# Optimization experiments

Hardware: AMD Instinct MI355X
Metric: run time of the kernel (lower is better)

## Reference

```python
import jax, jax.numpy as jnp
import numpy as np

B, S, D_IN, D_HID, D_OUT, PE_DIM = 8, 4096, 1024, 1024, 1024, 16


def sinusoidal_embeddings(batch_size, seq_len, dim):
    positions = jnp.arange(seq_len)[:, None].astype(jnp.float32)
    div_term = jnp.exp(jnp.arange(0, dim, 2).astype(jnp.float32) * (-jnp.log(10000.0) / dim))
    pe = jnp.zeros((seq_len, dim), dtype=jnp.float32)
    pe = pe.at[:, 0::2].set(jnp.sin(positions * div_term))
    pe = pe.at[:, 1::2].set(jnp.cos(positions * div_term))
    return jnp.broadcast_to(pe, (batch_size, seq_len, dim))


def setup_inputs() -> dict:
    key = jax.random.key(0)
    ks = jax.random.split(key, 8)
    d_cat = D_IN + PE_DIM
    # a_logit drawn so that sigmoid(a_logit) lands in the stable decay range [0.9, 0.999]
    u = jax.random.uniform(ks[1], (D_HID,), minval=0.9, maxval=0.999)
    a_logit = jnp.log(u) - jnp.log1p(-u)  # logit
    scale_in = 1.0 / np.sqrt(d_cat)
    scale_h = 1.0 / np.sqrt(D_HID)
    return {
        "x": jax.random.normal(ks[0], (B, S, D_IN), dtype=jnp.float32),
        "a_logit": a_logit.astype(jnp.float32),
        "W_dx": jax.random.normal(ks[2], (d_cat, D_OUT), dtype=jnp.float32) * scale_in,
        "b_dx": jnp.zeros((D_OUT,), dtype=jnp.float32),
        "W_in": jax.random.normal(ks[3], (d_cat, D_HID), dtype=jnp.float32) * scale_in,
        "b_in": jnp.zeros((D_HID,), dtype=jnp.float32),
        "W_out": jax.random.normal(ks[4], (D_HID, D_OUT), dtype=jnp.float32) * scale_h,
        "b_out": jnp.zeros((D_OUT,), dtype=jnp.float32),
    }


def reference(x, a_logit, W_dx, b_dx, W_in, b_in, W_out, b_out):
    batch, seq, _ = x.shape
    a = jax.nn.sigmoid(a_logit)  # (d_hidden,)
    # rnn_pos_embedding: concat 16-dim sinusoidal PE
    xc = jnp.concatenate([x, sinusoidal_embeddings(batch, seq, PE_DIM)], axis=-1)
    dx = xc @ W_dx + b_dx  # (B, S, d_out)
    u = xc @ W_in + b_in  # (B, S, d_hidden)
    # rnn_norm_input
    u = jnp.sqrt(1.0 - a ** 2) * u
    u = jnp.transpose(u, (1, 0, 2))  # (S, B, d_hidden)

    def step(h, xt):
        h = a * h + xt
        return h, h

    init = jnp.zeros((batch, a.shape[0]), dtype=x.dtype)
    _, h = jax.lax.scan(step, init, u)
    h = jnp.transpose(h, (1, 0, 2))  # (B, S, d_hidden)
    return (dx + h @ W_out + b_out) / 2
```

## Files before the change

kernel.cpp:

```cpp
#include <hip/hip_runtime.h>
#include <hip/hip_bf16.h>
#include <math.h>

#define B_DIM 8
#define S_DIM 4096
#define DIN   1024
#define DHID  1024
#define DOUT  1024
#define KCAT  1040
#define KC    1088
#define MTOT  (B_DIM*S_DIM)
#define NCHUNK 32
#define LCHUNK 128

typedef __attribute__((ext_vector_type(8))) short bf16x8;
typedef __attribute__((ext_vector_type(4))) float f32x4;
typedef __attribute__((ext_vector_type(4))) unsigned short u16x4;

__device__ __forceinline__ unsigned short f2bf(float f) {
  union { float f; unsigned u; } v; v.f = f;
  unsigned r = v.u + 0x7fffu + ((v.u >> 16) & 1u);
  return (unsigned short)(r >> 16);
}
__device__ __forceinline__ float bf2f(unsigned short h) {
  union { unsigned u; float f; } v; v.u = ((unsigned)h) << 16;
  return v.f;
}

#define GLOAD16(g, l)                                                         \
  __builtin_amdgcn_global_load_lds(                                           \
      (const __attribute__((address_space(1))) void*)(g),                     \
      (__attribute__((address_space(3))) void*)(l), 16, 0, 0)

#define BAR()   __builtin_amdgcn_s_barrier()
#define LGKM0() do { asm volatile("s_waitcnt lgkmcnt(0)" ::: "memory");       \
                     __builtin_amdgcn_sched_barrier(0); } while (0)


__global__ void prep_a_kernel(const float* __restrict__ logit,
                              float* __restrict__ avec, float* __restrict__ svec) {
  int d = blockIdx.x * 256 + threadIdx.x;
  if (d >= DHID) return;
  float a = 1.f / (1.f + expf(-logit[d]));
  avec[d] = a;
  svec[d] = sqrtf(fmaxf(0.f, 1.f - a * a));
}

__global__ __launch_bounds__(256) void transpose_cast_kernel(
    const float* __restrict__ W, unsigned short* __restrict__ Wt,
    int Ksrc, int KCdst) {
  __shared__ float tile[32][33];
  const int N = 1024;
  int kb = blockIdx.x * 32, nb = blockIdx.y * 32;
  int tx = threadIdx.x & 31, ty = threadIdx.x >> 5;
#pragma unroll
  for (int r = 0; r < 32; r += 8) {
    int k = kb + ty + r;
    tile[ty + r][tx] = (k < Ksrc) ? W[(size_t)k * N + nb + tx] : 0.f;
  }
  __syncthreads();
#pragma unroll
  for (int r = 0; r < 32; r += 8) {
    int n = nb + ty + r;
    Wt[(size_t)n * KCdst + kb + tx] = f2bf(tile[tx][ty + r]);
  }
}

__global__ __launch_bounds__(256) void build_xc_kernel(
    const float* __restrict__ x, unsigned short* __restrict__ xc) {
  int gid = blockIdx.x * 256 + threadIdx.x;
  if (gid >= MTOT * (KC / 4)) return;
  int row = gid / (KC / 4);
  int g = gid - row * (KC / 4);
  int col0 = g * 4;
  u16x4 val;
  if (col0 < DIN) {
    const float4 xv = *(const float4*)(x + (size_t)row * DIN + col0);
    val.x = f2bf(xv.x); val.y = f2bf(xv.y); val.z = f2bf(xv.z); val.w = f2bf(xv.w);
  } else {
    int t = row & (S_DIM - 1);
#pragma unroll
    for (int e = 0; e < 4; e++) {
      int col = col0 + e;
      float v = 0.f;
      if (col < KCAT) {
        int j = col - DIN;
        int i = j >> 1;
        float div = expf(-(float)i * 1.1512925465f);
        float arg = (float)t * div;
        v = (j & 1) ? cosf(arg) : sinf(arg);
      }
      val[e] = f2bf(v);
    }
  }
  *(u16x4*)(xc + (size_t)row * KC + col0) = val;
}


__device__ __forceinline__ bf16x8 frag(const unsigned short* hb, int row, int slot) {
  int ph = slot ^ (row & 7);
  return *(const bf16x8*)(hb + (size_t)row * 64 + ph * 8);
}

__device__ __forceinline__ void gemm_pipe2(
    const unsigned short* __restrict__ A,
    const unsigned short* __restrict__ Bt,
    int lda, int kt, int arow0, int brow0,
    unsigned short (*lA)[2][8192], unsigned short (*lB)[2][8192],
    f32x4 acc[8][4]) {
  const int tid = threadIdx.x;
  const int lane = tid & 63, w = tid >> 6;
  const int wrow = w >> 2, wcol = w & 3;
  const int rl = lane & 15, s = lane >> 4;

  const int c1 = tid, c2 = tid + 512;
  const int r1 = c1 >> 3, sl1 = (c1 & 7) ^ (r1 & 7);
  const int r2 = c2 >> 3, sl2 = (c2 & 7) ^ (r2 & 7);
  const unsigned short* pA1 = A + (size_t)(arow0 + r1) * lda + sl1 * 8;
  const unsigned short* pA2 = A + (size_t)(arow0 + r2) * lda + sl2 * 8;
  const unsigned short* pB1 = Bt + (size_t)(brow0 + r1) * lda + sl1 * 8;
  const unsigned short* pB2 = Bt + (size_t)(brow0 + r2) * lda + sl2 * 8;
  const size_t hstep = (size_t)128 * lda;

#define STG_A(t, h) do { size_t _o = (size_t)(t) * 64 + (size_t)(h) * hstep;  \
    int _b = (t) & 1;                                                         \
    GLOAD16(pA1 + _o, &lA[_b][h][(size_t)c1 * 8]);                            \
    GLOAD16(pA2 + _o, &lA[_b][h][(size_t)c2 * 8]); } while (0)
#define STG_B(t, h) do { size_t _o = (size_t)(t) * 64 + (size_t)(h) * hstep;  \
    int _b = (t) & 1;                                                         \
    GLOAD16(pB1 + _o, &lB[_b][h][(size_t)c1 * 8]);                            \
    GLOAD16(pB2 + _o, &lB[_b][h][(size_t)c2 * 8]); } while (0)

#define MFMA_Q(MH, NH, BB)                                                    \
  __builtin_amdgcn_s_setprio(1);                                              \
  _Pragma("unroll") for (int mq = 0; mq < 4; mq++)                            \
    _Pragma("unroll") for (int nq = 0; nq < 2; nq++)                          \
      _Pragma("unroll") for (int kk = 0; kk < 2; kk++)                        \
        acc[(MH)*4 + mq][(NH)*2 + nq] =                                       \
            __builtin_amdgcn_mfma_f32_16x16x32_bf16(                          \
                a[mq][kk], BB[nq][kk], acc[(MH)*4 + mq][(NH)*2 + nq], 0, 0, 0);\
  __builtin_amdgcn_s_setprio(0);

  STG_B(0, 0); STG_B(0, 1); STG_A(0, 0); STG_A(0, 1);
  STG_B(1, 0); STG_B(1, 1); STG_A(1, 0); STG_A(1, 1);
  asm volatile("s_waitcnt vmcnt(8)" ::: "memory");
  BAR();

  const int br = (wcol & 1) * 64;
  for (int t = 0; t < kt; ++t) {
    const bool st = (t + 2) < kt;
    const unsigned short* Ac = &lA[t & 1][wrow][0];
    const unsigned short* Bc = &lB[t & 1][wcol >> 1][0];
    bf16x8 a[4][2], b0[2][2], b1[2][2];

#pragma unroll
    for (int mq = 0; mq < 4; mq++)
#pragma unroll
      for (int kk = 0; kk < 2; kk++)
        a[mq][kk] = frag(Ac, mq * 16 + rl, kk * 4 + s);
#pragma unroll
    for (int nq = 0; nq < 2; nq++)
#pragma unroll
      for (int kk = 0; kk < 2; kk++)
        b0[nq][kk] = frag(Bc, br + nq * 16 + rl, kk * 4 + s);
    BAR(); LGKM0();
    MFMA_Q(0, 0, b0);
    BAR();

#pragma unroll
    for (int nq = 0; nq < 2; nq++)
#pragma unroll
      for (int kk = 0; kk < 2; kk++)
        b1[nq][kk] = frag(Bc, br + 32 + nq * 16 + rl, kk * 4 + s);
    BAR(); LGKM0();
    MFMA_Q(0, 1, b1);
    BAR();

#pragma unroll
    for (int mq = 0; mq < 4; mq++)
#pragma unroll
      for (int kk = 0; kk < 2; kk++)
        a[mq][kk] = frag(Ac, 64 + mq * 16 + rl, kk * 4 + s);
    if (st) { STG_B(t + 2, 0); STG_B(t + 2, 1); }
    BAR(); LGKM0();
    MFMA_Q(1, 1, b1);
    BAR();

    if (st) { STG_A(t + 2, 0); STG_A(t + 2, 1); }
    BAR();
    MFMA_Q(1, 0, b0);
    if (st) { asm volatile("s_waitcnt vmcnt(8)" ::: "memory"); }
    else    { asm volatile("s_waitcnt vmcnt(0)" ::: "memory"); }
    BAR();
  }
#undef STG_A
#undef STG_B
#undef MFMA_Q
}

__global__ __launch_bounds__(512, 2) void gemm_u_kernel(
    const unsigned short* __restrict__ xc, const unsigned short* __restrict__ Wtin,
    const float* __restrict__ b_in, const float* __restrict__ svec,
    unsigned short* __restrict__ u) {
  __shared__ __align__(16) unsigned short lA[2][2][8192];
  __shared__ __align__(16) unsigned short lB[2][2][8192];
  f32x4 acc[8][4];
  const f32x4 z = {0.f, 0.f, 0.f, 0.f};
#pragma unroll
  for (int i = 0; i < 8; i++)
#pragma unroll
    for (int n = 0; n < 4; n++) acc[i][n] = z;

  int bid = blockIdx.x;
  int swz = (bid & 7) * 64 + (bid >> 3);
  int bcol = swz >> 7, brow = swz & 127;

  gemm_pipe2(xc, Wtin, KC, KC / 64, brow * 256, bcol * 256, lA, lB, acc);

  const int lane = threadIdx.x & 63, w = threadIdx.x >> 6;
  const int wrow = w >> 2, wcol = w & 3;
  const int rl = lane & 15, s = lane >> 4;
  const int colb = bcol * 256 + wcol * 64 + rl;
  const int rowb = brow * 256 + wrow * 128 + s * 4;
#pragma unroll
  for (int n = 0; n < 4; n++) {
    int col = colb + n * 16;
    float bi = b_in[col], sv = svec[col];
#pragma unroll
    for (int i = 0; i < 8; i++) {
#pragma unroll
      for (int r = 0; r < 4; r++) {
        int row = rowb + i * 16 + r;
        u[(size_t)row * DHID + col] = f2bf((acc[i][n][r] + bi) * sv);
      }
    }
  }
}

__global__ __launch_bounds__(512, 2) void gemm_out_kernel(
    const unsigned short* __restrict__ xc, const unsigned short* __restrict__ Wtdx,
    const unsigned short* __restrict__ h, const unsigned short* __restrict__ Wtout,
    const float* __restrict__ b_dx, const float* __restrict__ b_out,
    float* __restrict__ out) {
  __shared__ __align__(16) unsigned short lA[2][2][8192];
  __shared__ __align__(16) unsigned short lB[2][2][8192];
  f32x4 acc[8][4];
  const f32x4 z = {0.f, 0.f, 0.f, 0.f};
#pragma unroll
  for (int i = 0; i < 8; i++)
#pragma unroll
    for (int n = 0; n < 4; n++) acc[i][n] = z;

  int bid = blockIdx.x;
  int swz = (bid & 7) * 64 + (bid >> 3);
  int bcol = swz >> 7, brow = swz & 127;

  gemm_pipe2(xc, Wtdx, KC, KC / 64, brow * 256, bcol * 256, lA, lB, acc);
  gemm_pipe2(h, Wtout, DHID, DHID / 64, brow * 256, bcol * 256, lA, lB, acc);

  const int lane = threadIdx.x & 63, w = threadIdx.x >> 6;
  const int wrow = w >> 2, wcol = w & 3;
  const int rl = lane & 15, s = lane >> 4;
  const int colb = bcol * 256 + wcol * 64 + rl;
  const int rowb = brow * 256 + wrow * 128 + s * 4;
#pragma unroll
  for (int n = 0; n < 4; n++) {
    int col = colb + n * 16;
    float bb = b_dx[col] + b_out[col];
#pragma unroll
    for (int i = 0; i < 8; i++) {
#pragma unroll
      for (int r = 0; r < 4; r++) {
        int row = rowb + i * 16 + r;
        out[(size_t)row * DOUT + col] = 0.5f * (acc[i][n][r] + bb);
      }
    }
  }
}


__global__ __launch_bounds__(256) void scan1_kernel(
    const float* __restrict__ avec, unsigned short* __restrict__ uh,
    float* __restrict__ carry) {
  int b = blockIdx.x >> 5, c = blockIdx.x & 31;
  int d0 = threadIdx.x * 4;
  float4 a4 = *(const float4*)(avec + d0);
  unsigned short* p = uh + ((size_t)(b * S_DIM + c * LCHUNK)) * DHID + d0;
  float h0 = 0.f, h1 = 0.f, h2 = 0.f, h3 = 0.f;
#pragma unroll 4
  for (int t = 0; t < LCHUNK; t++) {
    u16x4 v = *(u16x4*)(p + (size_t)t * DHID);
    h0 = fmaf(a4.x, h0, bf2f(v.x));
    h1 = fmaf(a4.y, h1, bf2f(v.y));
    h2 = fmaf(a4.z, h2, bf2f(v.z));
    h3 = fmaf(a4.w, h3, bf2f(v.w));
    v.x = f2bf(h0); v.y = f2bf(h1); v.z = f2bf(h2); v.w = f2bf(h3);
    *(u16x4*)(p + (size_t)t * DHID) = v;
  }
  float4 cv = {h0, h1, h2, h3};
  *(float4*)(carry + ((size_t)b * NCHUNK + c) * DHID + d0) = cv;
}

__global__ __launch_bounds__(256) void scan2_kernel(
    const float* __restrict__ avec, const float* __restrict__ carry,
    float* __restrict__ Hprev) {
  int gid = blockIdx.x * 256 + threadIdx.x;
  int b = gid >> 10, d = gid & 1023;
  float a = avec[d];
  float aL = a;
#pragma unroll
  for (int i = 0; i < 7; i++) aL *= aL;
  float H = 0.f;
#pragma unroll
  for (int c = 0; c < NCHUNK; c++) {
    size_t idx = ((size_t)b * NCHUNK + c) * DHID + d;
    Hprev[idx] = H;
    H = aL * H + carry[idx];
  }
}

__global__ __launch_bounds__(256) void scan3_kernel(
    const float* __restrict__ avec, unsigned short* __restrict__ uh,
    const float* __restrict__ Hprev) {
  int b = blockIdx.x >> 5, c = blockIdx.x & 31;
  int d0 = threadIdx.x * 4;
  float4 Hp = *(const float4*)(Hprev + ((size_t)b * NCHUNK + c) * DHID + d0);
  if (Hp.x == 0.f && Hp.y == 0.f && Hp.z == 0.f && Hp.w == 0.f) return;
  float4 a4 = *(const float4*)(avec + d0);
  float p0 = a4.x * Hp.x, p1 = a4.y * Hp.y, p2 = a4.z * Hp.z, p3 = a4.w * Hp.w;
  unsigned short* p = uh + ((size_t)(b * S_DIM + c * LCHUNK)) * DHID + d0;
#pragma unroll 4
  for (int t = 0; t < LCHUNK; t++) {
    u16x4 v = *(u16x4*)(p + (size_t)t * DHID);
    v.x = f2bf(bf2f(v.x) + p0);
    v.y = f2bf(bf2f(v.y) + p1);
    v.z = f2bf(bf2f(v.z) + p2);
    v.w = f2bf(bf2f(v.w) + p3);
    *(u16x4*)(p + (size_t)t * DHID) = v;
    p0 *= a4.x; p1 *= a4.y; p2 *= a4.z; p3 *= a4.w;
  }
}


extern "C" void kernel_launch(void* const* d_in, const int* in_sizes, int n_in,
                              void* d_out, int out_size, void* d_ws, size_t ws_size,
                              hipStream_t stream) {
  const float* x       = (const float*)d_in[0];
  const float* a_logit = (const float*)d_in[1];
  const float* W_dx    = (const float*)d_in[2];
  const float* b_dx    = (const float*)d_in[3];
  const float* W_in    = (const float*)d_in[4];
  const float* b_in    = (const float*)d_in[5];
  const float* W_out   = (const float*)d_in[6];
  const float* b_out   = (const float*)d_in[7];
  float* out = (float*)d_out;

  char* ws = (char*)d_ws;
  size_t off = 0;
  auto alloc = [&](size_t bytes) {
    void* p = ws + off;
    off += (bytes + 255) & ~(size_t)255;
    return p;
  };
  unsigned short* xc    = (unsigned short*)alloc((size_t)MTOT * KC * 2);
  unsigned short* Wtdx  = (unsigned short*)alloc((size_t)DOUT * KC * 2);
  unsigned short* Wtin  = (unsigned short*)alloc((size_t)DHID * KC * 2);
  unsigned short* Wtout = (unsigned short*)alloc((size_t)DOUT * DHID * 2);
  unsigned short* uh    = (unsigned short*)alloc((size_t)MTOT * DHID * 2);
  float* carry = (float*)alloc((size_t)B_DIM * NCHUNK * DHID * 4);
  float* Hprev = (float*)alloc((size_t)B_DIM * NCHUNK * DHID * 4);
  float* avec  = (float*)alloc(DHID * 4);
  float* svec  = (float*)alloc(DHID * 4);
  (void)ws_size; (void)in_sizes; (void)n_in; (void)out_size;

  prep_a_kernel<<<4, 256, 0, stream>>>(a_logit, avec, svec);
  transpose_cast_kernel<<<dim3(KC / 32, 32), 256, 0, stream>>>(W_dx, Wtdx, KCAT, KC);
  transpose_cast_kernel<<<dim3(KC / 32, 32), 256, 0, stream>>>(W_in, Wtin, KCAT, KC);
  transpose_cast_kernel<<<dim3(32, 32), 256, 0, stream>>>(W_out, Wtout, DHID, DHID);
  build_xc_kernel<<<(MTOT * (KC / 4) + 255) / 256, 256, 0, stream>>>(x, xc);

  gemm_u_kernel<<<512, 512, 0, stream>>>(xc, Wtin, b_in, svec, uh);

  scan1_kernel<<<B_DIM * NCHUNK, 256, 0, stream>>>(avec, uh, carry);
  scan2_kernel<<<32, 256, 0, stream>>>(avec, carry, Hprev);
  scan3_kernel<<<B_DIM * NCHUNK, 256, 0, stream>>>(avec, uh, Hprev);

  gemm_out_kernel<<<512, 512, 0, stream>>>(xc, Wtdx, uh, Wtout, b_dx, b_out, out);
}
```

Before: 339.6 us.

## Finer-grained LDS staging pipeline and fuse two GEMM segments into one loop

Replaces the two-stage pipeline with a schedule that stages each quarter tile (A lo/hi, B lo/hi) separately and spreads those loads across the four MFMA phases. The A-hi quarter for the next tile is fetched one step ahead, because the current A-hi half is still being read. In the output kernel, the dx and h@W_out GEMMs now run as one continuous K loop over two segments, which removes the pipeline drain and refill between them. The cost is per-stage segment-select logic and tighter vmcnt bookkeeping, which raises the risk of a race if a buffer is still in use when it is overwritten.

New measurement: 358.9 us. 1.06x slower.

```diff
diff --git a/kernel.cpp b/kernel.cpp
--- a/kernel.cpp
+++ b/kernel.cpp
@@ -102,100 +102,126 @@
   return *(const bf16x8*)(hb + (size_t)row * 64 + ph * 8);
 }
 
-__device__ __forceinline__ void gemm_pipe2(
-    const unsigned short* __restrict__ A,
-    const unsigned short* __restrict__ Bt,
-    int lda, int kt, int arow0, int brow0,
+#define READ_A4(dst, base, roff)                                              \
+  _Pragma("unroll") for (int mq = 0; mq < 4; mq++)                            \
+    _Pragma("unroll") for (int kk = 0; kk < 2; kk++)                          \
+      dst[mq][kk] = frag(base, (roff) + mq * 16 + rl, kk * 4 + s);
+
+#define READ_B2(dst, base, roff)                                              \
+  _Pragma("unroll") for (int nq = 0; nq < 2; nq++)                            \
+    _Pragma("unroll") for (int kk = 0; kk < 2; kk++)                          \
+      dst[nq][kk] = frag(base, (roff) + nq * 16 + rl, kk * 4 + s);
+
+#define MFMA_Q(MH, NH, AA, BB)                                                \
+  __builtin_amdgcn_s_setprio(1);                                              \
+  _Pragma("unroll") for (int mq = 0; mq < 4; mq++)                            \
+    _Pragma("unroll") for (int nq = 0; nq < 2; nq++)                          \
+      _Pragma("unroll") for (int kk = 0; kk < 2; kk++)                        \
+        acc[(MH)*4 + mq][(NH)*2 + nq] =                                       \
+            __builtin_amdgcn_mfma_f32_16x16x32_bf16(                          \
+                AA[mq][kk], BB[nq][kk], acc[(MH)*4 + mq][(NH)*2 + nq], 0,0,0);\
+  __builtin_amdgcn_s_setprio(0);
+
+template <int NSEG>
+__device__ __forceinline__ void gemm_pipe6(
+    const unsigned short* __restrict__ A0p, const unsigned short* __restrict__ B0p,
+    int lda0, int kt0,
+    const unsigned short* __restrict__ A1p, const unsigned short* __restrict__ B1p,
+    int lda1, int kt1,
+    int arow0, int brow0,
     unsigned short (*lA)[2][8192], unsigned short (*lB)[2][8192],
     f32x4 acc[8][4]) {
   const int tid = threadIdx.x;
   const int lane = tid & 63, w = tid >> 6;
   const int wrow = w >> 2, wcol = w & 3;
   const int rl = lane & 15, s = lane >> 4;
+  const int br = (wcol & 1) * 64;
+  const int kt = (NSEG == 2) ? (kt0 + kt1) : kt0;
 
   const int c1 = tid, c2 = tid + 512;
   const int r1 = c1 >> 3, sl1 = (c1 & 7) ^ (r1 & 7);
   const int r2 = c2 >> 3, sl2 = (c2 & 7) ^ (r2 & 7);
-  const unsigned short* pA1 = A + (size_t)(arow0 + r1) * lda + sl1 * 8;
-  const unsigned short* pA2 = A + (size_t)(arow0 + r2) * lda + sl2 * 8;
-  const unsigned short* pB1 = Bt + (size_t)(brow0 + r1) * lda + sl1 * 8;
-  const unsigned short* pB2 = Bt + (size_t)(brow0 + r2) * lda + sl2 * 8;
-  const size_t hstep = (size_t)128 * lda;
-
-#define STG_A(t, h) do { size_t _o = (size_t)(t) * 64 + (size_t)(h) * hstep;  \
-    int _b = (t) & 1;                                                         \
-    GLOAD16(pA1 + _o, &lA[_b][h][(size_t)c1 * 8]);                            \
-    GLOAD16(pA2 + _o, &lA[_b][h][(size_t)c2 * 8]); } while (0)
-#define STG_B(t, h) do { size_t _o = (size_t)(t) * 64 + (size_t)(h) * hstep;  \
-    int _b = (t) & 1;                                                         \
-    GLOAD16(pB1 + _o, &lB[_b][h][(size_t)c1 * 8]);                            \
-    GLOAD16(pB2 + _o, &lB[_b][h][(size_t)c2 * 8]); } while (0)
-
-#define MFMA_Q(MH, NH, BB)                                                    \
-  __builtin_amdgcn_s_setprio(1);                                              \
-  _Pragma("unroll") for (int mq = 0; mq < 4; mq++)                            \
-    _Pragma("unroll") for (int nq = 0; nq < 2; nq++)                          \
-      _Pragma("unroll") for (int kk = 0; kk < 2; kk++)                        \
-        acc[(MH)*4 + mq][(NH)*2 + nq] =                                       \
-            __builtin_amdgcn_mfma_f32_16x16x32_bf16(                          \
-                a[mq][kk], BB[nq][kk], acc[(MH)*4 + mq][(NH)*2 + nq], 0, 0, 0);\
-  __builtin_amdgcn_s_setprio(0);
-
-  STG_B(0, 0); STG_B(0, 1); STG_A(0, 0); STG_A(0, 1);
-  STG_B(1, 0); STG_B(1, 1); STG_A(1, 0); STG_A(1, 1);
-  asm volatile("s_waitcnt vmcnt(8)" ::: "memory");
+  const unsigned short* gA0lo = A0p + (size_t)(arow0 + r1) * lda0 + sl1 * 8;
+  const unsigned short* gA0hi = A0p + (size_t)(arow0 + r2) * lda0 + sl2 * 8;
+  const unsigned short* gB0lo = B0p + (size_t)(brow0 + r1) * lda0 + sl1 * 8;
+  const unsigned short* gB0hi = B0p + (size_t)(brow0 + r2) * lda0 + sl2 * 8;
+  const unsigned short* gA1lo = gA0lo; const unsigned short* gA1hi = gA0hi;
+  const unsigned short* gB1lo = gB0lo; const unsigned short* gB1hi = gB0hi;
+  if (NSEG == 2) {
+    gA1lo = A1p + (size_t)(arow0 + r1) * lda1 + sl1 * 8;
+    gA1hi = A1p + (size_t)(arow0 + r2) * lda1 + sl2 * 8;
+    gB1lo = B1p + (size_t)(brow0 + r1) * lda1 + sl1 * 8;
+    gB1hi = B1p + (size_t)(brow0 + r2) * lda1 + sl2 * 8;
+  }
+  const size_t hs0 = (size_t)128 * lda0, hs1 = (size_t)128 * lda1;
+
+  auto stgAlo = [&](int tt) {
+    const unsigned short* p = gA0lo; size_t hs = hs0; int rel = tt;
+    if (NSEG == 2 && tt >= kt0) { p = gA1lo; hs = hs1; rel = tt - kt0; }
+    p += (size_t)rel * 64;
+    GLOAD16(p,      &lA[tt & 1][0][(size_t)c1 * 8]);
+    GLOAD16(p + hs, &lA[tt & 1][1][(size_t)c1 * 8]);
+  };
+  auto stgAhi = [&](int tt) {
+    const unsigned short* p = gA0hi; size_t hs = hs0; int rel = tt;
+    if (NSEG == 2 && tt >= kt0) { p = gA1hi; hs = hs1; rel = tt - kt0; }
+    p += (size_t)rel * 64;
+    GLOAD16(p,      &lA[tt & 1][0][(size_t)c2 * 8]);
+    GLOAD16(p + hs, &lA[tt & 1][1][(size_t)c2 * 8]);
+  };
+  auto stgBlo = [&](int tt) {
+    const unsigned short* p = gB0lo; size_t hs = hs0; int rel = tt;
+    if (NSEG == 2 && tt >= kt0) { p = gB1lo; hs = hs1; rel = tt - kt0; }
+    p += (size_t)rel * 64;
+    GLOAD16(p,      &lB[tt & 1][0][(size_t)c1 * 8]);
+    GLOAD16(p + hs, &lB[tt & 1][1][(size_t)c1 * 8]);
+  };
+  auto stgBhi = [&](int tt) {
+    const unsigned short* p = gB0hi; size_t hs = hs0; int rel = tt;
+    if (NSEG == 2 && tt >= kt0) { p = gB1hi; hs = hs1; rel = tt - kt0; }
+    p += (size_t)rel * 64;
+    GLOAD16(p,      &lB[tt & 1][0][(size_t)c2 * 8]);
+    GLOAD16(p + hs, &lB[tt & 1][1][(size_t)c2 * 8]);
+  };
+
+  stgAlo(0); stgAhi(0); stgBlo(0); stgBhi(0);
+  stgAlo(1); stgBlo(1); stgBhi(1);
+  asm volatile("s_waitcnt vmcnt(6)" ::: "memory");
   BAR();
-
-  const int br = (wcol & 1) * 64;
+  __builtin_amdgcn_sched_barrier(0);
+
+#pragma unroll 2
   for (int t = 0; t < kt; ++t) {
-    const bool st = (t + 2) < kt;
     const unsigned short* Ac = &lA[t & 1][wrow][0];
     const unsigned short* Bc = &lB[t & 1][wcol >> 1][0];
-    bf16x8 a[4][2], b0[2][2], b1[2][2];
-
-#pragma unroll
-    for (int mq = 0; mq < 4; mq++)
-#pragma unroll
-      for (int kk = 0; kk < 2; kk++)
-        a[mq][kk] = frag(Ac, mq * 16 + rl, kk * 4 + s);
-#pragma unroll
-    for (int nq = 0; nq < 2; nq++)
-#pragma unroll
-      for (int kk = 0; kk < 2; kk++)
-        b0[nq][kk] = frag(Bc, br + nq * 16 + rl, kk * 4 + s);
+    bf16x8 alo[4][2], ahi[4][2], blo[2][2], bhi[2][2];
+
+    READ_A4(alo, Ac, 0);
+    READ_B2(blo, Bc, br);
+    if (t + 1 < kt) stgAhi(t + 1);
     BAR(); LGKM0();
-    MFMA_Q(0, 0, b0);
+    MFMA_Q(0, 0, alo, blo);
     BAR();
 
-#pragma unroll
-    for (int nq = 0; nq < 2; nq++)
-#pragma unroll
-      for (int kk = 0; kk < 2; kk++)
-        b1[nq][kk] = frag(Bc, br + 32 + nq * 16 + rl, kk * 4 + s);
+    READ_B2(bhi, Bc, br + 32);
+    if (t + 2 < kt) stgAlo(t + 2);
     BAR(); LGKM0();
-    MFMA_Q(0, 1, b1);
+    MFMA_Q(0, 1, alo, bhi);
     BAR();
 
-#pragma unroll
-    for (int mq = 0; mq < 4; mq++)
-#pragma unroll
-      for (int kk = 0; kk < 2; kk++)
-        a[mq][kk] = frag(Ac, 64 + mq * 16 + rl, kk * 4 + s);
-    if (st) { STG_B(t + 2, 0); STG_B(t + 2, 1); }
+    READ_A4(ahi, Ac, 64);
+    if (t + 2 < kt) stgBlo(t + 2);
     BAR(); LGKM0();
-    MFMA_Q(1, 1, b1);
+    MFMA_Q(1, 1, ahi, bhi);
     BAR();
 
-    if (st) { STG_A(t + 2, 0); STG_A(t + 2, 1); }
+    if (t + 2 < kt) stgBhi(t + 2);
     BAR();
-    MFMA_Q(1, 0, b0);
-    if (st) { asm volatile("s_waitcnt vmcnt(8)" ::: "memory"); }
-    else    { asm volatile("s_waitcnt vmcnt(0)" ::: "memory"); }
+    MFMA_Q(1, 0, ahi, blo);
+    if (t + 2 < kt)      { asm volatile("s_waitcnt vmcnt(6)" ::: "memory"); }
+    else if (t + 1 < kt) { asm volatile("s_waitcnt vmcnt(0)" ::: "memory"); }
     BAR();
   }
-#undef STG_A
-#undef STG_B
-#undef MFMA_Q
 }
 
 __global__ __launch_bounds__(512, 2) void gemm_u_kernel(
@@ -215,7 +241,8 @@
   int swz = (bid & 7) * 64 + (bid >> 3);
   int bcol = swz >> 7, brow = swz & 127;
 
-  gemm_pipe2(xc, Wtin, KC, KC / 64, brow * 256, bcol * 256, lA, lB, acc);
+  gemm_pipe6<1>(xc, Wtin, KC, KC / 64, xc, Wtin, KC, 0,
+                brow * 256, bcol * 256, lA, lB, acc);
 
   const int lane = threadIdx.x & 63, w = threadIdx.x >> 6;
   const int wrow = w >> 2, wcol = w & 3;
@@ -255,8 +282,8 @@
   int swz = (bid & 7) * 64 + (bid >> 3);
   int bcol = swz >> 7, brow = swz & 127;
 
-  gemm_pipe2(xc, Wtdx, KC, KC / 64, brow * 256, bcol * 256, lA, lB, acc);
-  gemm_pipe2(h, Wtout, DHID, DHID / 64, brow * 256, bcol * 256, lA, lB, acc);
+  gemm_pipe6<2>(xc, Wtdx, KC, KC / 64, h, Wtout, DHID, DHID / 64,
+                brow * 256, bcol * 256, lA, lB, acc);
 
   const int lane = threadIdx.x & 63, w = threadIdx.x >> 6;
   const int wrow = w >> 2, wcol = w & 3;
```

## Fuse three-pass chunked scan into one kernel with last-block carry propagation

Applied to the files above, without the earlier changes.

Replaces the scan1/scan2/scan3 kernel sequence with a single kernel. The first pass only reads uh to compute chunk carries and no longer writes it back. The last block of each batch, detected through an atomic counter, computes the prefix carries and releases the other blocks through a flag. Each block then rescans its chunk from the correct initial state and writes uh once, which removes one full write pass and two launches. The price is a spin-wait on the flag, which needs all 256 blocks to be co-resident (likely on this GPU), plus an extra memset launch.

Result: slower. 463.6 us (+36.5%).

```diff
diff --git a/kernel.cpp b/kernel.cpp
--- a/kernel.cpp
+++ b/kernel.cpp
@@ -102,6 +102,17 @@
   return *(const bf16x8*)(hb + (size_t)row * 64 + ph * 8);
 }
 
+#define MFMA_Q(MH, NH, BB)                                                    \
+  __builtin_amdgcn_s_setprio(1);                                              \
+  _Pragma("unroll") for (int mq = 0; mq < 4; mq++)                            \
+    _Pragma("unroll") for (int nq = 0; nq < 2; nq++)                          \
+      _Pragma("unroll") for (int kk = 0; kk < 2; kk++)                        \
+        acc[(MH)*4 + mq][(NH)*2 + nq] =                                       \
+            __builtin_amdgcn_mfma_f32_16x16x32_bf16(                          \
+                a[kk == 0 ? mq : mq][kk], BB[nq][kk],                         \
+                acc[(MH)*4 + mq][(NH)*2 + nq], 0, 0, 0);                      \
+  __builtin_amdgcn_s_setprio(0);
+
 __device__ __forceinline__ void gemm_pipe2(
     const unsigned short* __restrict__ A,
     const unsigned short* __restrict__ Bt,
@@ -131,16 +142,6 @@
     GLOAD16(pB1 + _o, &lB[_b][h][(size_t)c1 * 8]);                            \
     GLOAD16(pB2 + _o, &lB[_b][h][(size_t)c2 * 8]); } while (0)
 
-#define MFMA_Q(MH, NH, BB)                                                    \
-  __builtin_amdgcn_s_setprio(1);                                              \
-  _Pragma("unroll") for (int mq = 0; mq < 4; mq++)                            \
-    _Pragma("unroll") for (int nq = 0; nq < 2; nq++)                          \
-      _Pragma("unroll") for (int kk = 0; kk < 2; kk++)                        \
-        acc[(MH)*4 + mq][(NH)*2 + nq] =                                       \
-            __builtin_amdgcn_mfma_f32_16x16x32_bf16(                          \
-                a[mq][kk], BB[nq][kk], acc[(MH)*4 + mq][(NH)*2 + nq], 0, 0, 0);\
-  __builtin_amdgcn_s_setprio(0);
-
   STG_B(0, 0); STG_B(0, 1); STG_A(0, 0); STG_A(0, 1);
   STG_B(1, 0); STG_B(1, 1); STG_A(1, 0); STG_A(1, 1);
   asm volatile("s_waitcnt vmcnt(8)" ::: "memory");
@@ -195,7 +196,6 @@
   }
 #undef STG_A
 #undef STG_B
-#undef MFMA_Q
 }
 
 __global__ __launch_bounds__(512, 2) void gemm_u_kernel(
@@ -279,65 +279,89 @@
 }
 
 
-__global__ __launch_bounds__(256) void scan1_kernel(
+__global__ __launch_bounds__(256) void scan_fused_kernel(
     const float* __restrict__ avec, unsigned short* __restrict__ uh,
-    float* __restrict__ carry) {
+    float* __restrict__ carry, float* __restrict__ Hprev,
+    int* __restrict__ cnt, int* __restrict__ go) {
   int b = blockIdx.x >> 5, c = blockIdx.x & 31;
   int d0 = threadIdx.x * 4;
   float4 a4 = *(const float4*)(avec + d0);
   unsigned short* p = uh + ((size_t)(b * S_DIM + c * LCHUNK)) * DHID + d0;
+
   float h0 = 0.f, h1 = 0.f, h2 = 0.f, h3 = 0.f;
 #pragma unroll 4
   for (int t = 0; t < LCHUNK; t++) {
-    u16x4 v = *(u16x4*)(p + (size_t)t * DHID);
+    u16x4 v = *(const u16x4*)(p + (size_t)t * DHID);
     h0 = fmaf(a4.x, h0, bf2f(v.x));
     h1 = fmaf(a4.y, h1, bf2f(v.y));
     h2 = fmaf(a4.z, h2, bf2f(v.z));
     h3 = fmaf(a4.w, h3, bf2f(v.w));
-    v.x = f2bf(h0); v.y = f2bf(h1); v.z = f2bf(h2); v.w = f2bf(h3);
-    *(u16x4*)(p + (size_t)t * DHID) = v;
-  }
-  float4 cv = {h0, h1, h2, h3};
-  *(float4*)(carry + ((size_t)b * NCHUNK + c) * DHID + d0) = cv;
-}
-
-__global__ __launch_bounds__(256) void scan2_kernel(
-    const float* __restrict__ avec, const float* __restrict__ carry,
-    float* __restrict__ Hprev) {
-  int gid = blockIdx.x * 256 + threadIdx.x;
-  int b = gid >> 10, d = gid & 1023;
-  float a = avec[d];
-  float aL = a;
-#pragma unroll
-  for (int i = 0; i < 7; i++) aL *= aL;
-  float H = 0.f;
-#pragma unroll
-  for (int c = 0; c < NCHUNK; c++) {
-    size_t idx = ((size_t)b * NCHUNK + c) * DHID + d;
-    Hprev[idx] = H;
-    H = aL * H + carry[idx];
-  }
-}
-
-__global__ __launch_bounds__(256) void scan3_kernel(
-    const float* __restrict__ avec, unsigned short* __restrict__ uh,
-    const float* __restrict__ Hprev) {
-  int b = blockIdx.x >> 5, c = blockIdx.x & 31;
-  int d0 = threadIdx.x * 4;
-  float4 Hp = *(const float4*)(Hprev + ((size_t)b * NCHUNK + c) * DHID + d0);
-  if (Hp.x == 0.f && Hp.y == 0.f && Hp.z == 0.f && Hp.w == 0.f) return;
-  float4 a4 = *(const float4*)(avec + d0);
-  float p0 = a4.x * Hp.x, p1 = a4.y * Hp.y, p2 = a4.z * Hp.z, p3 = a4.w * Hp.w;
-  unsigned short* p = uh + ((size_t)(b * S_DIM + c * LCHUNK)) * DHID + d0;
+  }
+  size_t cidx = ((size_t)b * NCHUNK + c) * DHID + d0;
+  __hip_atomic_store(&carry[cidx + 0], h0, __ATOMIC_RELAXED, __HIP_MEMORY_SCOPE_AGENT);
+  __hip_atomic_store(&carry[cidx + 1], h1, __ATOMIC_RELAXED, __HIP_MEMORY_SCOPE_AGENT);
+  __hip_atomic_store(&carry[cidx + 2], h2, __ATOMIC_RELAXED, __HIP_MEMORY_SCOPE_AGENT);
+  __hip_atomic_store(&carry[cidx + 3], h3, __ATOMIC_RELAXED, __HIP_MEMORY_SCOPE_AGENT);
+  __threadfence();
+  __syncthreads();
+
+  __shared__ int amI;
+  if (threadIdx.x == 0) {
+    int old = __hip_atomic_fetch_add(&cnt[b], 1, __ATOMIC_ACQ_REL,
+                                     __HIP_MEMORY_SCOPE_AGENT);
+    amI = (old == NCHUNK - 1);
+  }
+  __syncthreads();
+
+  float H0, H1, H2, H3;
+  if (amI) {
+    float aL0 = a4.x, aL1 = a4.y, aL2 = a4.z, aL3 = a4.w;
+#pragma unroll
+    for (int i = 0; i < 7; i++) { aL0 *= aL0; aL1 *= aL1; aL2 *= aL2; aL3 *= aL3; }
+    float G0 = 0.f, G1 = 0.f, G2 = 0.f, G3 = 0.f;
+    float m0 = 0.f, m1 = 0.f, m2 = 0.f, m3 = 0.f;
+    for (int cc = 0; cc < NCHUNK; cc++) {
+      size_t idx = ((size_t)b * NCHUNK + cc) * DHID + d0;
+      if (cc == c) { m0 = G0; m1 = G1; m2 = G2; m3 = G3; }
+      __hip_atomic_store(&Hprev[idx + 0], G0, __ATOMIC_RELAXED, __HIP_MEMORY_SCOPE_AGENT);
+      __hip_atomic_store(&Hprev[idx + 1], G1, __ATOMIC_RELAXED, __HIP_MEMORY_SCOPE_AGENT);
+      __hip_atomic_store(&Hprev[idx + 2], G2, __ATOMIC_RELAXED, __HIP_MEMORY_SCOPE_AGENT);
+      __hip_atomic_store(&Hprev[idx + 3], G3, __ATOMIC_RELAXED, __HIP_MEMORY_SCOPE_AGENT);
+      float r0 = __hip_atomic_load(&carry[idx + 0], __ATOMIC_RELAXED, __HIP_MEMORY_SCOPE_AGENT);
+      float r1 = __hip_atomic_load(&carry[idx + 1], __ATOMIC_RELAXED, __HIP_MEMORY_SCOPE_AGENT);
+      float r2 = __hip_atomic_load(&carry[idx + 2], __ATOMIC_RELAXED, __HIP_MEMORY_SCOPE_AGENT);
+      float r3 = __hip_atomic_load(&carry[idx + 3], __ATOMIC_RELAXED, __HIP_MEMORY_SCOPE_AGENT);
+      G0 = fmaf(aL0, G0, r0); G1 = fmaf(aL1, G1, r1);
+      G2 = fmaf(aL2, G2, r2); G3 = fmaf(aL3, G3, r3);
+    }
+    __threadfence();
+    __syncthreads();
+    if (threadIdx.x == 0)
+      __hip_atomic_store(&go[b], 1, __ATOMIC_RELEASE, __HIP_MEMORY_SCOPE_AGENT);
+    H0 = m0; H1 = m1; H2 = m2; H3 = m3;
+  } else {
+    if (threadIdx.x == 0) {
+      while (__hip_atomic_load(&go[b], __ATOMIC_ACQUIRE,
+                               __HIP_MEMORY_SCOPE_AGENT) == 0)
+        __builtin_amdgcn_s_sleep(8);
+    }
+    __syncthreads();
+    size_t idx = ((size_t)b * NCHUNK + c) * DHID + d0;
+    H0 = __hip_atomic_load(&Hprev[idx + 0], __ATOMIC_RELAXED, __HIP_MEMORY_SCOPE_AGENT);
+    H1 = __hip_atomic_load(&Hprev[idx + 1], __ATOMIC_RELAXED, __HIP_MEMORY_SCOPE_AGENT);
+    H2 = __hip_atomic_load(&Hprev[idx + 2], __ATOMIC_RELAXED, __HIP_MEMORY_SCOPE_AGENT);
+    H3 = __hip_atomic_load(&Hprev[idx + 3], __ATOMIC_RELAXED, __HIP_MEMORY_SCOPE_AGENT);
+  }
+
 #pragma unroll 4
   for (int t = 0; t < LCHUNK; t++) {
-    u16x4 v = *(u16x4*)(p + (size_t)t * DHID);
-    v.x = f2bf(bf2f(v.x) + p0);
-    v.y = f2bf(bf2f(v.y) + p1);
-    v.z = f2bf(bf2f(v.z) + p2);
-    v.w = f2bf(bf2f(v.w) + p3);
+    u16x4 v = *(const u16x4*)(p + (size_t)t * DHID);
+    H0 = fmaf(a4.x, H0, bf2f(v.x));
+    H1 = fmaf(a4.y, H1, bf2f(v.y));
+    H2 = fmaf(a4.z, H2, bf2f(v.z));
+    H3 = fmaf(a4.w, H3, bf2f(v.w));
+    v.x = f2bf(H0); v.y = f2bf(H1); v.z = f2bf(H2); v.w = f2bf(H3);
     *(u16x4*)(p + (size_t)t * DHID) = v;
-    p0 *= a4.x; p1 *= a4.y; p2 *= a4.z; p3 *= a4.w;
   }
 }
 
@@ -371,8 +395,10 @@
   float* Hprev = (float*)alloc((size_t)B_DIM * NCHUNK * DHID * 4);
   float* avec  = (float*)alloc(DHID * 4);
   float* svec  = (float*)alloc(DHID * 4);
+  int*   flags = (int*)alloc(16 * 4);
   (void)ws_size; (void)in_sizes; (void)n_in; (void)out_size;
 
+  hipMemsetAsync(flags, 0, 16 * 4, stream);
   prep_a_kernel<<<4, 256, 0, stream>>>(a_logit, avec, svec);
   transpose_cast_kernel<<<dim3(KC / 32, 32), 256, 0, stream>>>(W_dx, Wtdx, KCAT, KC);
   transpose_cast_kernel<<<dim3(KC / 32, 32), 256, 0, stream>>>(W_in, Wtin, KCAT, KC);
@@ -381,9 +407,8 @@
 
   gemm_u_kernel<<<512, 512, 0, stream>>>(xc, Wtin, b_in, svec, uh);
 
-  scan1_kernel<<<B_DIM * NCHUNK, 256, 0, stream>>>(avec, uh, carry);
-  scan2_kernel<<<32, 256, 0, stream>>>(avec, carry, Hprev);
-  scan3_kernel<<<B_DIM * NCHUNK, 256, 0, stream>>>(avec, uh, Hprev);
+  scan_fused_kernel<<<B_DIM * NCHUNK, 256, 0, stream>>>(avec, uh, carry, Hprev,
+                                                        flags, flags + 8);
 
   gemm_out_kernel<<<512, 512, 0, stream>>>(xc, Wtdx, uh, Wtout, b_dx, b_out, out);
 }
```
